# Performance work log

Hardware: AMD Instinct MI355X
Metric: run time of the kernel (lower is better)

The kernel has to match this reference:

```python
import jax, jax.numpy as jnp
import numpy as np

G, N, E = 4, 20000, 320000
D_IN = 512
# ceil(0.6*N), ceil(0.6*K1), ceil(0.5*K2) -- SAGPooling ratios 0.6, 0.6, 0.5
K1, K2, K3 = 12000, 7200, 3600
EPS = 1e-5


def setup_inputs() -> dict:
    key = jax.random.key(0)
    ks = jax.random.split(key, 32)
    def w(k, shape, fan_in):
        return jax.random.normal(k, shape, jnp.float32) / np.float32(np.sqrt(fan_in))
    inp = {
        "x": jax.random.normal(ks[0], (G, N, D_IN), jnp.float32),
        "edge_index": jax.random.randint(ks[1], (G, 2, E), 0, N, dtype=jnp.int32),
        # GCNConv weights (lin has no bias; bias added post-aggregation)
        "W1": w(ks[2], (512, 512), 512), "b1": jnp.zeros((512,), jnp.float32),
        "W2": w(ks[3], (512, 512), 512), "b2": jnp.zeros((512,), jnp.float32),
        "W3": w(ks[4], (512, 256), 512), "b3": jnp.zeros((256,), jnp.float32),
        "W4": w(ks[5], (256, 256), 256), "b4": jnp.zeros((256,), jnp.float32),
        # BatchNorm (track_running_stats=False -> always batch stats), affine params
        "g1": jnp.ones((512,), jnp.float32), "be1": jnp.zeros((512,), jnp.float32),
        "g2": jnp.ones((512,), jnp.float32), "be2": jnp.zeros((512,), jnp.float32),
        "g3": jnp.ones((256,), jnp.float32), "be3": jnp.zeros((256,), jnp.float32),
        # SAGPooling score GNN = GraphConv(d, 1): lin_rel (with bias) + lin_root (no bias)
        "p1_wrel": w(ks[6], (512, 1), 512), "p1_brel": jnp.zeros((1,), jnp.float32), "p1_wroot": w(ks[7], (512, 1), 512),
        "p2_wrel": w(ks[8], (512, 1), 512), "p2_brel": jnp.zeros((1,), jnp.float32), "p2_wroot": w(ks[9], (512, 1), 512),
        "p3_wrel": w(ks[10], (256, 1), 256), "p3_brel": jnp.zeros((1,), jnp.float32), "p3_wroot": w(ks[11], (256, 1), 256),
        "lin_w": w(ks[12], (256, 256), 256), "lin_b": jnp.zeros((256,), jnp.float32),
        "lin2_w": w(ks[13], (256, 1), 256), "lin2_b": jnp.zeros((1,), jnp.float32),
    }
    return inp


def _gcn(x, src, dst, w, W, b, n):
    # GCNConv, add_self_loops=False: deg from edge weights on target, sym-norm messages
    deg = jax.ops.segment_sum(w, dst, num_segments=n)
    dinv = jnp.where(deg > 0, jax.lax.rsqrt(jnp.where(deg > 0, deg, 1.0)), 0.0)
    norm = w * dinv[src] * dinv[dst]                       # [E]
    h = x @ W                                              # [n, d_out]
    return jax.ops.segment_sum(norm[:, None] * h[src], dst, num_segments=n) + b


def _bn(x, g, b):
    mu = jnp.mean(x, axis=0)
    var = jnp.mean((x - mu) ** 2, axis=0)
    return (x - mu) * jax.lax.rsqrt(var + EPS) * g + b


def _sag_pool(x, src, dst, w, wrel, brel, wroot, n, k):
    # score GNN = GraphConv: lin_rel(sum_j w_e x_j) + lin_root(x_i); tanh nonlinearity
    agg = jax.ops.segment_sum(w[:, None] * x[src], dst, num_segments=n)
    score = jnp.tanh((agg @ wrel + brel + x @ wroot)[:, 0])  # [n]
    top, perm = jax.lax.top_k(score, k)
    x2 = x[perm] * top[:, None]
    # filter_adj: keep edges with both endpoints selected, re-index; modeled via mask
    mapping = jnp.full((n,), -1, jnp.int32).at[perm].set(jnp.arange(k, dtype=jnp.int32))
    s2, d2 = mapping[src], mapping[dst]
    valid = (s2 >= 0) & (d2 >= 0) & (w > 0)
    return x2, jnp.maximum(s2, 0), jnp.maximum(d2, 0), valid.astype(x.dtype)


def _per_graph(x, src, dst, p):
    w = jnp.ones((E,), x.dtype)
    h = jax.nn.relu(_bn(_gcn(x, src, dst, w, p["W1"], p["b1"], N), p["g1"], p["be1"]))
    h, src, dst, w = _sag_pool(h, src, dst, w, p["p1_wrel"], p["p1_brel"], p["p1_wroot"], N, K1)
    h = jax.nn.relu(_bn(_gcn(h, src, dst, w, p["W2"], p["b2"], K1), p["g2"], p["be2"]))
    h, src, dst, w = _sag_pool(h, src, dst, w, p["p2_wrel"], p["p2_brel"], p["p2_wroot"], K1, K2)
    h = jax.nn.relu(_bn(_gcn(h, src, dst, w, p["W3"], p["b3"], K2), p["g3"], p["be3"]))
    h, src, dst, w = _sag_pool(h, src, dst, w, p["p3_wrel"], p["p3_brel"], p["p3_wroot"], K2, K3)
    h = _gcn(h, src, dst, w, p["W4"], p["b4"], K3)
    return jnp.max(h, axis=0)                               # global_max_pool, 1 graph/data


def reference(x, edge_index, W1, b1, W2, b2, W3, b3, W4, b4,
              g1, be1, g2, be2, g3, be3,
              p1_wrel, p1_brel, p1_wroot, p2_wrel, p2_brel, p2_wroot,
              p3_wrel, p3_brel, p3_wroot, lin_w, lin_b, lin2_w, lin2_b):
    p = dict(W1=W1, b1=b1, W2=W2, b2=b2, W3=W3, b3=b3, W4=W4, b4=b4,
             g1=g1, be1=be1, g2=g2, be2=be2, g3=g3, be3=be3,
             p1_wrel=p1_wrel, p1_brel=p1_brel, p1_wroot=p1_wroot,
             p2_wrel=p2_wrel, p2_brel=p2_brel, p2_wroot=p2_wroot,
             p3_wrel=p3_wrel, p3_brel=p3_brel, p3_wroot=p3_wroot)
    feats = [_per_graph(x[g], edge_index[g, 0], edge_index[g, 1], p) for g in range(G)]
    wsi = jnp.stack(feats, axis=0)                          # [G, 256] (each data has 1 graph)
    x1 = jnp.mean(wsi, axis=0, keepdims=True)               # [1, 256]
    out = jax.nn.relu(x1 @ lin_w + lin_b) @ lin2_w + lin2_b # [1, 1]
    return (out, x1)
```

## Files before the change

### kernel.cpp

```cpp
#include <hip/hip_runtime.h>

#define NGRAPH 4
#define N0 20000
#define EDG 320000
#define KP1 12000
#define KP2 7200
#define KP3 3600

typedef unsigned short u16;
typedef unsigned int u32;
typedef unsigned long long u64;
typedef short s16x8 __attribute__((ext_vector_type(8)));
typedef u16 u16x4 __attribute__((ext_vector_type(4)));
typedef u16 u16x8 __attribute__((ext_vector_type(8)));
typedef float f32x4 __attribute__((ext_vector_type(4)));

__device__ __forceinline__ float b2f(u16 v){ return __uint_as_float(((u32)v)<<16); }
__device__ __forceinline__ u16 f2bf(float f){
  u32 u=__float_as_uint(f); u32 r=(u + 0x7FFFu + ((u>>16)&1u))>>16; return (u16)r;
}

__global__ void k_probe(float* dout, int n, float code){
  int i = blockIdx.x*256 + threadIdx.x;
  if (i >= n) return;
  dout[i] = (i == 0) ? code : 12345.0f;
}

__global__ void k_zero_i32(int* p, int n){
  int i = blockIdx.x*256 + threadIdx.x;
  if (i < n) p[i] = 0;
}

__global__ void k_castw2(const float* W, u16* Wth, u16* Wtl, int K, int N){
  __shared__ float tile[32][33];
  int k0 = blockIdx.x*32, n0 = blockIdx.y*32;
  int tx = threadIdx.x & 31, ty = threadIdx.x >> 5;
  for (int r = ty; r < 32; r += 8)
    tile[r][tx] = W[(long)(k0+r)*N + n0 + tx];
  __syncthreads();
  for (int r = ty; r < 32; r += 8){
    float v = tile[tx][r];
    u16 hi = f2bf(v);
    float rs = v - b2f(hi);
    Wth[(long)(n0+r)*K + k0 + tx] = hi;
    Wtl[(long)(n0+r)*K + k0 + tx] = f2bf(rs);
  }
}

__global__ void k_edges_init(const int* ei, int* esrc, int* edst){
  int idx = blockIdx.x*256 + threadIdx.x;
  if (idx >= NGRAPH*EDG) return;
  int g = idx / EDG, e = idx - g*EDG;
  esrc[idx] = ei[(g*2+0)*EDG + e];
  edst[idx] = ei[(g*2+1)*EDG + e];
}

__global__ void k_deg(const int* esrc, const int* edst, int* deg, int n){
  int idx = blockIdx.x*256 + threadIdx.x;
  if (idx >= NGRAPH*EDG) return;
  int s = esrc[idx];
  if (s < 0) return;
  atomicAdd(&deg[(idx/EDG)*n + edst[idx]], 1);
}

__global__ void k_dinv(const int* deg, float* dinv, int ntot){
  int i = blockIdx.x*256 + threadIdx.x;
  if (i >= ntot) return;
  int d = deg[i];
  dinv[i] = (d > 0) ? rsqrtf((float)d) : 0.0f;
}

__global__ __launch_bounds__(1024) void k_scan1(const int* deg, int* offs, int* bsum, int n){
  int tid = threadIdx.x;
  int i = blockIdx.x*1024 + tid;
  __shared__ int buf[1024];
  int v = (i < n) ? deg[i] : 0;
  buf[tid] = v;
  __syncthreads();
  for (int off = 1; off < 1024; off <<= 1){
    int xv = (tid >= off) ? buf[tid-off] : 0;
    __syncthreads();
    buf[tid] += xv;
    __syncthreads();
  }
  if (i < n) offs[i] = buf[tid] - v;
  if (tid == 1023) bsum[blockIdx.x] = buf[1023];
}

__global__ __launch_bounds__(128) void k_scan2(int* bsum, int* offs, int nb, int n){
  int t = threadIdx.x;
  int v = (t < nb) ? bsum[t] : 0;
  __shared__ int buf[128];
  buf[t] = v;
  __syncthreads();
  for (int off = 1; off < 128; off <<= 1){
    int x = (t >= off) ? buf[t-off] : 0;
    __syncthreads();
    buf[t] += x;
    __syncthreads();
  }
  if (t < nb) bsum[t] = buf[t] - v;
  if (t == 127) offs[n] = buf[127];
}

__global__ __launch_bounds__(1024) void k_scan3(int* offs, const int* bsum, int n){
  int i = blockIdx.x*1024 + threadIdx.x;
  if (i < n) offs[i] += bsum[blockIdx.x];
}

__global__ void k_copy_i32(const int* a, int* b, int n){
  int i = blockIdx.x*256 + threadIdx.x;
  if (i < n) b[i] = a[i];
}

__global__ void k_csrfill(const int* esrc, const int* edst, const float* dinv,
                          int* cursor, int* csr_src, float* csr_norm, int n){
  int idx = blockIdx.x*256 + threadIdx.x;
  if (idx >= NGRAPH*EDG) return;
  int s = esrc[idx];
  if (s < 0) return;
  int g = idx/EDG;
  int d = edst[idx];
  int gs = g*n + s, gd = g*n + d;
  int pos = atomicAdd(&cursor[gd], 1);
  csr_src[pos] = gs;
  csr_norm[pos] = dinv[gs]*dinv[gd];
}

__global__ __launch_bounds__(256) void k_gemm3(const float* A, const u16* Bh_, const u16* Bl_,
                                               float* C, int K, int Nc){
  __shared__ u16 Ah[128][40];
  __shared__ u16 Al[128][40];
  __shared__ u16 Bh[128][40];
  __shared__ u16 Bl[128][40];
  const int n0 = blockIdx.x*128, m0 = blockIdx.y*128;
  const int tid = threadIdx.x, w = tid>>6, lane = tid&63;
  const int wr = w>>1, wc = w&1;
  const int fr = lane&15, fq = lane>>4;
  const int ar = tid>>3, ac = (tid&7)*4;
  const int br = tid>>2, bc = (tid&3)*8;
  f32x4 acc[4][4];
  #pragma unroll
  for (int i=0;i<4;++i)
    #pragma unroll
    for (int j=0;j<4;++j){ acc[i][j][0]=0.f; acc[i][j][1]=0.f; acc[i][j][2]=0.f; acc[i][j][3]=0.f; }
  for (int k0 = 0; k0 < K; k0 += 32){
    __syncthreads();
    #pragma unroll
    for (int i = 0; i < 4; ++i){
      int row = ar + i*32;
      float4 av = *(const float4*)(A + (long)(m0+row)*K + k0 + ac);
      float vs[4] = {av.x, av.y, av.z, av.w};
      u16x4 h, l;
      #pragma unroll
      for (int j = 0; j < 4; ++j){
        u16 hi = f2bf(vs[j]);
        h[j] = hi;
        l[j] = f2bf(vs[j] - b2f(hi));
      }
      *(u16x4*)&Ah[row][ac] = h;
      *(u16x4*)&Al[row][ac] = l;
    }
    #pragma unroll
    for (int i = 0; i < 2; ++i){
      int row = br + i*64;
      *(u16x8*)&Bh[row][bc] = *(const u16x8*)(Bh_ + (long)(n0+row)*K + k0 + bc);
      *(u16x8*)&Bl[row][bc] = *(const u16x8*)(Bl_ + (long)(n0+row)*K + k0 + bc);
    }
    __syncthreads();
    s16x8 fah[4], fal[4], fbh[4], fbl[4];
    #pragma unroll
    for (int fm = 0; fm < 4; ++fm){
      fah[fm] = *(const s16x8*)&Ah[wr*64 + fm*16 + fr][fq*8];
      fal[fm] = *(const s16x8*)&Al[wr*64 + fm*16 + fr][fq*8];
    }
    #pragma unroll
    for (int fn = 0; fn < 4; ++fn){
      fbh[fn] = *(const s16x8*)&Bh[wc*64 + fn*16 + fr][fq*8];
      fbl[fn] = *(const s16x8*)&Bl[wc*64 + fn*16 + fr][fq*8];
    }
    #pragma unroll
    for (int fm = 0; fm < 4; ++fm)
      #pragma unroll
      for (int fn = 0; fn < 4; ++fn){
        acc[fm][fn] = __builtin_amdgcn_mfma_f32_16x16x32_bf16(fal[fm], fbh[fn], acc[fm][fn], 0, 0, 0);
        acc[fm][fn] = __builtin_amdgcn_mfma_f32_16x16x32_bf16(fah[fm], fbl[fn], acc[fm][fn], 0, 0, 0);
        acc[fm][fn] = __builtin_amdgcn_mfma_f32_16x16x32_bf16(fah[fm], fbh[fn], acc[fm][fn], 0, 0, 0);
      }
  }
  #pragma unroll
  for (int fm = 0; fm < 4; ++fm){
    const int r0 = m0 + wr*64 + fm*16 + fq*4;
    #pragma unroll
    for (int fn = 0; fn < 4; ++fn){
      const int c0 = n0 + wc*64 + fn*16 + fr;
      #pragma unroll
      for (int r = 0; r < 4; ++r)
        C[(long)(r0+r)*Nc + c0] = acc[fm][fn][r];
    }
  }
}

template<int D>
__global__ void k_agg(const float* hW, const int* offs, const int* deg,
                      const int* csr_src, const float* csr_norm,
                      const float* bias, float* out, int ntot){
  int node = blockIdx.x*4 + (threadIdx.x>>6);
  if (node >= ntot) return;
  int lane = threadIdx.x & 63;
  const int V = D/256;
  f32x4 acc[V];
  #pragma unroll
  for (int j=0;j<V;++j){ acc[j][0]=0.f; acc[j][1]=0.f; acc[j][2]=0.f; acc[j][3]=0.f; }
  int p0 = offs[node], p1 = p0 + deg[node];
  for (int p = p0; p < p1; ++p) {
    int src = csr_src[p];
    float nm = csr_norm[p];
    const float* row = hW + (long)src*D + lane*4;
    #pragma unroll
    for (int j=0;j<V;++j){
      f32x4 v = *(const f32x4*)(row + j*256);
      acc[j] += nm*v;
    }
  }
  float* orow = out + (long)node*D + lane*4;
  const float* brow = bias + lane*4;
  #pragma unroll
  for (int j=0;j<V;++j){
    f32x4 b = *(const f32x4*)(brow + j*256);
    *(f32x4*)(orow + j*256) = acc[j] + b;
  }
}

template<int D>
__global__ void k_bnpart(const float* h, float* part, int n, int NB){
  int g = blockIdx.y, bx = blockIdx.x;
  int r0 = bx*256;
  int rows = n - r0; if (rows > 256) rows = 256;
  const int CPT = D/256;
  float s[CPT], q[CPT];
  #pragma unroll
  for (int j=0;j<CPT;++j){ s[j]=0.0f; q[j]=0.0f; }
  const float* base = h + ((long)g*n + r0)*D;
  for (int r = 0; r < rows; ++r)
    #pragma unroll
    for (int j=0;j<CPT;++j){
      float v = base[(long)r*D + threadIdx.x + j*256];
      s[j] += v; q[j] += v*v;
    }
  float* o = part + ((long)(g*NB + bx)*2)*D;
  #pragma unroll
  for (int j=0;j<CPT;++j){
    o[threadIdx.x + j*256]     = s[j];
    o[D + threadIdx.x + j*256] = q[j];
  }
}

__global__ void k_bnfin(const float* part, float* mean, float* rstd, int n, int D, int NB){
  int idx = blockIdx.x*256 + threadIdx.x;
  if (idx >= NGRAPH*D) return;
  int g = idx / D, c = idx - g*D;
  float s = 0.0f, q = 0.0f;
  for (int b = 0; b < NB; ++b){
    const float* o = part + ((long)(g*NB + b)*2)*D;
    s += o[c]; q += o[D + c];
  }
  float m = s/(float)n;
  float v = q/(float)n - m*m;
  mean[idx] = m;
  rstd[idx] = rsqrtf(v + 1e-5f);
}

template<int D>
__global__ void k_bnrelu_dots(float* h, const float* mean, const float* rstd,
                              const float* gam, const float* bet,
                              const float* wrel, const float* wroot,
                              float* r, float* t, int n, int ntot){
  int node = blockIdx.x*4 + (threadIdx.x>>6);
  if (node >= ntot) return;
  int lane = threadIdx.x & 63;
  int g = node / n;
  const float* mu = mean + g*D;
  const float* rs = rstd + g*D;
  float* row = h + (long)node*D;
  float sr = 0.0f, st = 0.0f;
  #pragma unroll
  for (int j = 0; j < D/64; ++j){
    int c = lane + j*64;
    float v = (row[c] - mu[c])*rs[c]*gam[c] + bet[c];
    v = fmaxf(v, 0.0f);
    row[c] = v;
    sr += v*wrel[c];
    st += v*wroot[c];
  }
  for (int o = 32; o > 0; o >>= 1){
    sr += __shfl_down(sr, o);
    st += __shfl_down(st, o);
  }
  if (lane == 0){ r[node] = sr; t[node] = st; }
}

__global__ void k_score(const float* r, const float* t, const int* offs, const int* deg,
                        const int* csr_src, const float* brel, float* score,
                        u64* keys, int n, int ntot){
  int i = blockIdx.x*256 + threadIdx.x;
  if (i >= ntot) return;
  float a = 0.0f;
  int p0 = offs[i], p1 = p0 + deg[i];
  for (int p = p0; p < p1; ++p) a += r[csr_src[p]];
  float sc = tanhf(a + brel[0] + t[i]);
  score[i] = sc;
  u32 u = __float_as_uint(sc);
  u = (u & 0x80000000u) ? ~u : (u | 0x80000000u);
  keys[i] = ((u64)u << 32) | (u64)(0xFFFFFFFFu - (u32)(i % n));
}

__global__ __launch_bounds__(1024) void k_radix(const u64* keys, u64* Tout, int n, int k){
  int g = blockIdx.x;
  const u64* kk = keys + (long)g*n;
  __shared__ u32 h0[2048];
  __shared__ u32 h1[2048];
  __shared__ u64 s_prefix;
  __shared__ int s_remaining;
  __shared__ int s_bin;
  if (threadIdx.x == 0){ s_prefix = 0ull; s_remaining = k; }
  int consumed = 0;
  for (int round = 0; round < 6; ++round){
    int nb = (round < 5) ? 11 : 9;
    int shift = 64 - consumed - nb;
    int bins = 1 << nb;
    for (int i = threadIdx.x; i < bins; i += 1024) h0[i] = 0u;
    __syncthreads();
    u64 pref = s_prefix;
    int rem = s_remaining;
    for (int i = threadIdx.x; i < n; i += 1024){
      u64 key = kk[i];
      if (consumed == 0 || (key >> (64 - consumed)) == pref)
        atomicAdd(&h0[(u32)((key >> shift) & (u64)(bins-1))], 1u);
    }
    __syncthreads();
    u32* src = h0; u32* dst = h1;
    for (int off = 1; off < bins; off <<= 1){
      for (int i = threadIdx.x; i < bins; i += 1024)
        dst[i] = src[i] + ((i + off < bins) ? src[i + off] : 0u);
      __syncthreads();
      u32* tmp = src; src = dst; dst = tmp;
    }
    for (int i = threadIdx.x; i < bins; i += 1024){
      int Sb  = (int)src[i];
      int Sb1 = (i + 1 < bins) ? (int)src[i+1] : 0;
      if (Sb >= rem && (i == bins-1 || Sb1 < rem)){
        s_bin = i;
        s_remaining = rem - Sb1;
      }
    }
    __syncthreads();
    if (threadIdx.x == 0) s_prefix = (s_prefix << nb) | (u64)s_bin;
    consumed += nb;
    __syncthreads();
  }
  if (threadIdx.x == 0) Tout[g] = s_prefix;
}

__global__ void k_select(const u64* keys, const u64* T, int* mapping,
                         int* perm, int* cnt, int n, int k, int ntot){
  int gi = blockIdx.x*256 + threadIdx.x;
  int lane = threadIdx.x & 63;
  if (gi - lane >= ntot) return;
  int g = gi / n;
  bool sel = keys[gi] >= T[g];
  u64 ball = __ballot(sel);
  u64 lt = (1ull << lane) - 1ull;
  int g0 = __shfl(g, 0);
  u64 sameg = __ballot(g == g0);
  int id = -1;
  if (g == g0){
    u64 mA = ball & sameg;
    int baseA = 0;
    if (lane == 0 && mA) baseA = atomicAdd(&cnt[g0], __popcll(mA));
    baseA = __shfl(baseA, 0);
    if (sel) id = baseA + __popcll(mA & lt);
  } else {
    u64 blanes = ~sameg;
    int firstB = (int)(__ffsll((long long)blanes) - 1);
    u64 mB = ball & blanes;
    int baseB = 0;
    if (lane == firstB && mB) baseB = atomicAdd(&cnt[g], __popcll(mB));
    baseB = __shfl(baseB, firstB);
    if (sel) id = baseB + __popcll(mB & lt);
  }
  mapping[gi] = id;
  if (id >= 0) perm[g*k + id] = gi - g*n;
}

__global__ void k_poolcopy(const float* h, const float* score, const int* perm,
                           float* outA, int n, int k, int D, int mtot){
  int m = blockIdx.x*4 + (threadIdx.x>>6);
  if (m >= mtot) return;
  int lane = threadIdx.x & 63;
  int g = m / k;
  int gi = g*n + perm[m];
  float sc = score[gi];
  const float* row = h + (long)gi*D;
  float* orow = outA + (long)m*D;
  for (int c = lane; c < D; c += 64) orow[c] = row[c]*sc;
}

__global__ void k_remap(int* esrc, int* edst, const int* mapping, int n){
  int idx = blockIdx.x*256 + threadIdx.x;
  if (idx >= NGRAPH*EDG) return;
  int s = esrc[idx];
  if (s < 0) return;
  int g = idx/EDG;
  int s2 = mapping[g*n + s], d2 = mapping[g*n + edst[idx]];
  if (s2 < 0 || d2 < 0){ esrc[idx] = -1; edst[idx] = -1; }
  else { esrc[idx] = s2; edst[idx] = d2; }
}

__global__ void k_maxpart(const float* h, float* part){
  int g = blockIdx.y, b = blockIdx.x, c = threadIdx.x;
  int r0 = b*240;
  const float* base = h + ((long)g*KP3 + r0)*256;
  float m = -3.4e38f;
  for (int r = 0; r < 240; ++r) m = fmaxf(m, base[(long)r*256 + c]);
  part[(g*15 + b)*256 + c] = m;
}

__global__ void k_maxfin(const float* part, float* feats){
  int g = blockIdx.x, c = threadIdx.x;
  float m = -3.4e38f;
  for (int b = 0; b < 15; ++b) m = fmaxf(m, part[(g*15 + b)*256 + c]);
  feats[g*256 + c] = m;
}

__global__ void k_final(const float* feats, const float* lw, const float* lb,
                        const float* l2w, const float* l2b, float* dout){
  __shared__ float sx[256];
  __shared__ float sp[256];
  int c = threadIdx.x;
  float x1 = 0.25f*(feats[c] + feats[256+c] + feats[512+c] + feats[768+c]);
  sx[c] = x1;
  __syncthreads();
  float acc = lb[c];
  for (int j = 0; j < 256; ++j) acc += sx[j]*lw[j*256 + c];
  acc = fmaxf(acc, 0.0f);
  sp[c] = acc*l2w[c];
  __syncthreads();
  for (int off = 128; off > 0; off >>= 1){
    if (c < off) sp[c] += sp[c+off];
    __syncthreads();
  }
  if (c == 0) dout[0] = sp[0] + l2b[0];
  dout[1+c] = sx[c];
}

extern "C" void kernel_launch(void* const* d_in, const int* in_sizes, int n_in,
                              void* d_out, int out_size, void* d_ws, size_t ws_size,
                              hipStream_t stream){
  const float* x  = (const float*)d_in[0];
  const int*   ei = (const int*)d_in[1];
  const float *W1 = (const float*)d_in[2],  *b1 = (const float*)d_in[3];
  const float *W2 = (const float*)d_in[4],  *b2 = (const float*)d_in[5];
  const float *W3 = (const float*)d_in[6],  *b3 = (const float*)d_in[7];
  const float *W4 = (const float*)d_in[8],  *b4 = (const float*)d_in[9];
  const float *g1 = (const float*)d_in[10], *be1 = (const float*)d_in[11];
  const float *g2 = (const float*)d_in[12], *be2 = (const float*)d_in[13];
  const float *g3 = (const float*)d_in[14], *be3 = (const float*)d_in[15];
  const float *p1r = (const float*)d_in[16], *p1b = (const float*)d_in[17], *p1o = (const float*)d_in[18];
  const float *p2r = (const float*)d_in[19], *p2b = (const float*)d_in[20], *p2o = (const float*)d_in[21];
  const float *p3r = (const float*)d_in[22], *p3b = (const float*)d_in[23], *p3o = (const float*)d_in[24];
  const float *lw = (const float*)d_in[25], *lb = (const float*)d_in[26];
  const float *l2w = (const float*)d_in[27], *l2b = (const float*)d_in[28];
  float* dout = (float*)d_out;

  bool ok = (n_in == 29) && (out_size == 257)
         && (in_sizes[0] == NGRAPH*N0*512) && (in_sizes[1] == NGRAPH*2*EDG);
  float code = ok ? (float)(ws_size >> 20) : 7777777.0f;
  k_probe<<<2,256,0,stream>>>(dout, out_size, code);
  if (!ok) return;

  char* wbase = (char*)d_ws;
  size_t woff = 0;
  auto alloc = [&](size_t bytes) -> void* {
    void* p = wbase + woff;
    woff = (woff + bytes + 255) & ~(size_t)255;
    return p;
  };
  size_t NE = (size_t)NGRAPH*N0;
  size_t RSZ = NE*512*4;
  float* R0 = (float*)alloc(RSZ);
  float* R1 = (float*)alloc(RSZ);
  u16* Wt1h = (u16*)alloc((size_t)512*512*2); u16* Wt1l = (u16*)alloc((size_t)512*512*2);
  u16* Wt2h = (u16*)alloc((size_t)512*512*2); u16* Wt2l = (u16*)alloc((size_t)512*512*2);
  u16* Wt3h = (u16*)alloc((size_t)256*512*2); u16* Wt3l = (u16*)alloc((size_t)256*512*2);
  u16* Wt4h = (u16*)alloc((size_t)256*256*2); u16* Wt4l = (u16*)alloc((size_t)256*256*2);
  int*   esrc     = (int*)  alloc((size_t)NGRAPH*EDG*4);
  int*   edst     = (int*)  alloc((size_t)NGRAPH*EDG*4);
  int*   csr_src  = (int*)  alloc((size_t)NGRAPH*EDG*4);
  float* csr_norm = (float*)alloc((size_t)NGRAPH*EDG*4);
  int*   deg      = (int*)  alloc(NE*4);
  float* dinv     = (float*)alloc(NE*4);
  int*   offs     = (int*)  alloc((NE+1)*4);
  int*   cursor   = (int*)  alloc(NE*4);
  int*   bsum     = (int*)  alloc(128*4);
  float* rbuf     = (float*)alloc(NE*4);
  float* tbuf     = (float*)alloc(NE*4);
  float* sbuf     = (float*)alloc(NE*4);
  u64*   keys     = (u64*)  alloc(NE*8);
  u64*   Tsel     = (u64*)  alloc(NGRAPH*8);
  int*   cnt      = (int*)  alloc(NGRAPH*4);
  int*   mapping  = (int*)  alloc(NE*4);
  int*   perm     = (int*)  alloc((size_t)NGRAPH*KP1*4);
  float* bnpart   = (float*)alloc((size_t)NGRAPH*79*2*512*4);
  float* bnmean   = (float*)alloc((size_t)NGRAPH*512*4);
  float* bnrstd   = (float*)alloc((size_t)NGRAPH*512*4);
  float* maxpart  = (float*)alloc((size_t)NGRAPH*15*256*4);
  float* feats    = (float*)alloc((size_t)NGRAPH*256*4);

  auto cdiv = [](long a, long b) -> int { return (int)((a + b - 1)/b); };
  long etot = (long)NGRAPH*EDG;

  {
    dim3 g1d(512/32, 512/32);
    k_castw2<<<g1d,256,0,stream>>>(W1, Wt1h, Wt1l, 512, 512);
    k_castw2<<<g1d,256,0,stream>>>(W2, Wt2h, Wt2l, 512, 512);
    dim3 g3d(512/32, 256/32);
    k_castw2<<<g3d,256,0,stream>>>(W3, Wt3h, Wt3l, 512, 256);
    dim3 g4d(256/32, 256/32);
    k_castw2<<<g4d,256,0,stream>>>(W4, Wt4h, Wt4l, 256, 256);
  }
  k_edges_init<<<cdiv(etot,256),256,0,stream>>>(ei, esrc, edst);

  struct SP { int n, din, dout_, knext; const u16 *Wh,*Wl; const float *b,*gam,*bet,*wrel,*brel,*wroot; };
  SP sp[4] = {
    {N0,  512, 512, KP1, Wt1h,Wt1l, b1,g1,be1,p1r,p1b,p1o},
    {KP1, 512, 512, KP2, Wt2h,Wt2l, b2,g2,be2,p2r,p2b,p2o},
    {KP2, 512, 256, KP3, Wt3h,Wt3l, b3,g3,be3,p3r,p3b,p3o},
    {KP3, 256, 256, 0,   Wt4h,Wt4l, b4,0,0,0,0,0},
  };

  float* bufA = R0;
  float* bufB = R1;

  for (int s = 0; s < 4; ++s){
    SP& P = sp[s];
    int ntot = NGRAPH*P.n;
    int D = P.dout_;
    const float* Ain = (s == 0) ? x : bufA;
    float* H = bufB;
    float* C = bufA;

    k_zero_i32<<<cdiv(ntot,256),256,0,stream>>>(deg, ntot);
    k_deg<<<cdiv(etot,256),256,0,stream>>>(esrc, edst, deg, P.n);
    k_dinv<<<cdiv(ntot,256),256,0,stream>>>(deg, dinv, ntot);
    {
      int nb = cdiv(ntot, 1024);
      k_scan1<<<nb,1024,0,stream>>>(deg, offs, bsum, ntot);
      k_scan2<<<1,128,0,stream>>>(bsum, offs, nb, ntot);
      k_scan3<<<nb,1024,0,stream>>>(offs, bsum, ntot);
    }
    k_copy_i32<<<cdiv(ntot,256),256,0,stream>>>(offs, cursor, ntot);
    k_csrfill<<<cdiv(etot,256),256,0,stream>>>(esrc, edst, dinv, cursor, csr_src, csr_norm, P.n);
    {
      dim3 gg(D/128, cdiv(ntot,128));
      k_gemm3<<<gg,256,0,stream>>>(Ain, P.Wh, P.Wl, H, P.din, D);
    }
    if (D == 512)
      hipLaunchKernelGGL(HIP_KERNEL_NAME(k_agg<512>), dim3(ntot/4), dim3(256), 0, stream,
                         H, offs, deg, csr_src, csr_norm, P.b, C, ntot);
    else
      hipLaunchKernelGGL(HIP_KERNEL_NAME(k_agg<256>), dim3(ntot/4), dim3(256), 0, stream,
                         H, offs, deg, csr_src, csr_norm, P.b, C, ntot);
    if (s < 3){
      int NB = cdiv(P.n, 256);
      if (D == 512)
        hipLaunchKernelGGL(HIP_KERNEL_NAME(k_bnpart<512>), dim3(NB,NGRAPH), dim3(256), 0, stream,
                           C, bnpart, P.n, NB);
      else
        hipLaunchKernelGGL(HIP_KERNEL_NAME(k_bnpart<256>), dim3(NB,NGRAPH), dim3(256), 0, stream,
                           C, bnpart, P.n, NB);
      k_bnfin<<<cdiv((long)NGRAPH*D,256),256,0,stream>>>(bnpart, bnmean, bnrstd, P.n, D, NB);
      if (D == 512)
        hipLaunchKernelGGL(HIP_KERNEL_NAME(k_bnrelu_dots<512>), dim3(ntot/4), dim3(256), 0, stream,
                           C, bnmean, bnrstd, P.gam, P.bet, P.wrel, P.wroot, rbuf, tbuf, P.n, ntot);
      else
        hipLaunchKernelGGL(HIP_KERNEL_NAME(k_bnrelu_dots<256>), dim3(ntot/4), dim3(256), 0, stream,
                           C, bnmean, bnrstd, P.gam, P.bet, P.wrel, P.wroot, rbuf, tbuf, P.n, ntot);
      k_score<<<cdiv(ntot,256),256,0,stream>>>(rbuf, tbuf, offs, deg, csr_src, P.brel, sbuf, keys, P.n, ntot);
      k_radix<<<NGRAPH,1024,0,stream>>>(keys, Tsel, P.n, P.knext);
      k_zero_i32<<<1,64,0,stream>>>(cnt, NGRAPH);
      k_select<<<cdiv(ntot,256),256,0,stream>>>(keys, Tsel, mapping, perm, cnt, P.n, P.knext, ntot);
      int mtot = NGRAPH*P.knext;
      k_poolcopy<<<mtot/4,256,0,stream>>>(C, sbuf, perm, bufB, P.n, P.knext, D, mtot);
      k_remap<<<cdiv(etot,256),256,0,stream>>>(esrc, edst, mapping, P.n);
      float* tmp = bufA; bufA = bufB; bufB = tmp;
    } else {
      k_maxpart<<<dim3(15,NGRAPH),256,0,stream>>>(C, maxpart);
      k_maxfin<<<NGRAPH,256,0,stream>>>(maxpart, feats);
      k_final<<<1,256,0,stream>>>(feats, lw, lb, l2w, l2b, dout);
    }
  }
}
```

Before: 1.883 ms.

## Derive pooled-graph CSR by filtering previous CSR instead of rebuilding from edges

```diff
diff --git a/kernel.cpp b/kernel.cpp
--- a/kernel.cpp
+++ b/kernel.cpp
@@ -58,23 +58,16 @@
 __global__ void k_deg(const int* esrc, const int* edst, int* deg, int n){
   int idx = blockIdx.x*256 + threadIdx.x;
   if (idx >= NGRAPH*EDG) return;
-  int s = esrc[idx];
-  if (s < 0) return;
   atomicAdd(&deg[(idx/EDG)*n + edst[idx]], 1);
 }
 
-__global__ void k_dinv(const int* deg, float* dinv, int ntot){
-  int i = blockIdx.x*256 + threadIdx.x;
-  if (i >= ntot) return;
-  int d = deg[i];
-  dinv[i] = (d > 0) ? rsqrtf((float)d) : 0.0f;
-}
-
-__global__ __launch_bounds__(1024) void k_scan1(const int* deg, int* offs, int* bsum, int n){
+__global__ __launch_bounds__(1024) void k_scan1(const int* deg, int* offs, int* bsum,
+                                                float* dinv, int n){
   int tid = threadIdx.x;
   int i = blockIdx.x*1024 + tid;
   __shared__ int buf[1024];
   int v = (i < n) ? deg[i] : 0;
+  if (i < n) dinv[i] = (v > 0) ? rsqrtf((float)v) : 0.0f;
   buf[tid] = v;
   __syncthreads();
   for (int off = 1; off < 1024; off <<= 1){
@@ -117,14 +110,47 @@
                           int* cursor, int* csr_src, float* csr_norm, int n){
   int idx = blockIdx.x*256 + threadIdx.x;
   if (idx >= NGRAPH*EDG) return;
-  int s = esrc[idx];
-  if (s < 0) return;
   int g = idx/EDG;
-  int d = edst[idx];
-  int gs = g*n + s, gd = g*n + d;
+  int gs = g*n + esrc[idx], gd = g*n + edst[idx];
   int pos = atomicAdd(&cursor[gd], 1);
   csr_src[pos] = gs;
   csr_norm[pos] = dinv[gs]*dinv[gd];
+}
+
+__global__ void k_filterdeg(const int* perm, const int* mapping,
+                            const int* offs_o, const int* deg_o, const int* csrs_o,
+                            int* deg_n, int n_old, int k, int mtot){
+  int m = blockIdx.x*256 + threadIdx.x;
+  if (m >= mtot) return;
+  int g = m / k;
+  int gio = g*n_old + perm[m];
+  int p0 = offs_o[gio], p1 = p0 + deg_o[gio];
+  int c = 0;
+  for (int p = p0; p < p1; ++p)
+    if (mapping[csrs_o[p]] >= 0) ++c;
+  deg_n[m] = c;
+}
+
+__global__ void k_filterfill(const int* perm, const int* mapping,
+                             const int* offs_o, const int* deg_o, const int* csrs_o,
+                             const int* offs_n, const float* dinv_n,
+                             int* csrs_n, float* csrn_n, int n_old, int k, int mtot){
+  int m = blockIdx.x*256 + threadIdx.x;
+  if (m >= mtot) return;
+  int g = m / k;
+  int gio = g*n_old + perm[m];
+  int p0 = offs_o[gio], p1 = p0 + deg_o[gio];
+  int pos = offs_n[m];
+  float dd = dinv_n[m];
+  for (int p = p0; p < p1; ++p){
+    int sm = mapping[csrs_o[p]];
+    if (sm >= 0){
+      int sg = g*k + sm;
+      csrs_n[pos] = sg;
+      csrn_n[pos] = dinv_n[sg]*dd;
+      ++pos;
+    }
+  }
 }
 
 __global__ __launch_bounds__(256) void k_gemm3(const float* A, const u16* Bh_, const u16* Bl_,
@@ -406,17 +432,6 @@
   for (int c = lane; c < D; c += 64) orow[c] = row[c]*sc;
 }
 
-__global__ void k_remap(int* esrc, int* edst, const int* mapping, int n){
-  int idx = blockIdx.x*256 + threadIdx.x;
-  if (idx >= NGRAPH*EDG) return;
-  int s = esrc[idx];
-  if (s < 0) return;
-  int g = idx/EDG;
-  int s2 = mapping[g*n + s], d2 = mapping[g*n + edst[idx]];
-  if (s2 < 0 || d2 < 0){ esrc[idx] = -1; edst[idx] = -1; }
-  else { esrc[idx] = s2; edst[idx] = d2; }
-}
-
 __global__ void k_maxpart(const float* h, float* part){
   int g = blockIdx.y, b = blockIdx.x, c = threadIdx.x;
   int r0 = b*240;
@@ -494,28 +509,32 @@
   u16* Wt2h = (u16*)alloc((size_t)512*512*2); u16* Wt2l = (u16*)alloc((size_t)512*512*2);
   u16* Wt3h = (u16*)alloc((size_t)256*512*2); u16* Wt3l = (u16*)alloc((size_t)256*512*2);
   u16* Wt4h = (u16*)alloc((size_t)256*256*2); u16* Wt4l = (u16*)alloc((size_t)256*256*2);
-  int*   esrc     = (int*)  alloc((size_t)NGRAPH*EDG*4);
-  int*   edst     = (int*)  alloc((size_t)NGRAPH*EDG*4);
-  int*   csr_src  = (int*)  alloc((size_t)NGRAPH*EDG*4);
-  float* csr_norm = (float*)alloc((size_t)NGRAPH*EDG*4);
-  int*   deg      = (int*)  alloc(NE*4);
-  float* dinv     = (float*)alloc(NE*4);
-  int*   offs     = (int*)  alloc((NE+1)*4);
-  int*   cursor   = (int*)  alloc(NE*4);
-  int*   bsum     = (int*)  alloc(128*4);
-  float* rbuf     = (float*)alloc(NE*4);
-  float* tbuf     = (float*)alloc(NE*4);
-  float* sbuf     = (float*)alloc(NE*4);
-  u64*   keys     = (u64*)  alloc(NE*8);
-  u64*   Tsel     = (u64*)  alloc(NGRAPH*8);
-  int*   cnt      = (int*)  alloc(NGRAPH*4);
-  int*   mapping  = (int*)  alloc(NE*4);
-  int*   perm     = (int*)  alloc((size_t)NGRAPH*KP1*4);
-  float* bnpart   = (float*)alloc((size_t)NGRAPH*79*2*512*4);
-  float* bnmean   = (float*)alloc((size_t)NGRAPH*512*4);
-  float* bnrstd   = (float*)alloc((size_t)NGRAPH*512*4);
-  float* maxpart  = (float*)alloc((size_t)NGRAPH*15*256*4);
-  float* feats    = (float*)alloc((size_t)NGRAPH*256*4);
+  int*   esrc  = (int*)alloc((size_t)NGRAPH*EDG*4);
+  int*   edst  = (int*)alloc((size_t)NGRAPH*EDG*4);
+  int*   csrsA = (int*)  alloc((size_t)NGRAPH*EDG*4);
+  float* csrnA = (float*)alloc((size_t)NGRAPH*EDG*4);
+  int*   csrsB = (int*)  alloc((size_t)NGRAPH*EDG*4);
+  float* csrnB = (float*)alloc((size_t)NGRAPH*EDG*4);
+  int*   degA  = (int*)  alloc(NE*4);
+  int*   degB  = (int*)  alloc(NE*4);
+  int*   offsA = (int*)  alloc((NE+1)*4);
+  int*   offsB = (int*)  alloc((NE+1)*4);
+  float* dinv  = (float*)alloc(NE*4);
+  int*   cursor= (int*)  alloc(NE*4);
+  int*   bsum  = (int*)  alloc(128*4);
+  float* rbuf  = (float*)alloc(NE*4);
+  float* tbuf  = (float*)alloc(NE*4);
+  float* sbuf  = (float*)alloc(NE*4);
+  u64*   keys  = (u64*)  alloc(NE*8);
+  u64*   Tsel  = (u64*)  alloc(NGRAPH*8);
+  int*   cnt   = (int*)  alloc(NGRAPH*4);
+  int*   mapping = (int*)alloc(NE*4);
+  int*   perm  = (int*)  alloc((size_t)NGRAPH*KP1*4);
+  float* bnpart= (float*)alloc((size_t)NGRAPH*79*2*512*4);
+  float* bnmean= (float*)alloc((size_t)NGRAPH*512*4);
+  float* bnrstd= (float*)alloc((size_t)NGRAPH*512*4);
+  float* maxpart=(float*)alloc((size_t)NGRAPH*15*256*4);
+  float* feats = (float*)alloc((size_t)NGRAPH*256*4);
 
   auto cdiv = [](long a, long b) -> int { return (int)((a + b - 1)/b); };
   long etot = (long)NGRAPH*EDG;
@@ -542,6 +561,11 @@
   float* bufA = R0;
   float* bufB = R1;
 
+  int *deg_c = degA, *offs_c = offsA, *csrs_c = csrsA;
+  float *csrn_c = csrnA;
+  int *deg_x = degB, *offs_x = offsB, *csrs_x = csrsB;
+  float *csrn_x = csrnB;
+
   for (int s = 0; s < 4; ++s){
     SP& P = sp[s];
     int ntot = NGRAPH*P.n;
@@ -549,28 +573,42 @@
     const float* Ain = (s == 0) ? x : bufA;
     float* H = bufB;
     float* C = bufA;
-
-    k_zero_i32<<<cdiv(ntot,256),256,0,stream>>>(deg, ntot);
-    k_deg<<<cdiv(etot,256),256,0,stream>>>(esrc, edst, deg, P.n);
-    k_dinv<<<cdiv(ntot,256),256,0,stream>>>(deg, dinv, ntot);
-    {
-      int nb = cdiv(ntot, 1024);
-      k_scan1<<<nb,1024,0,stream>>>(deg, offs, bsum, ntot);
-      k_scan2<<<1,128,0,stream>>>(bsum, offs, nb, ntot);
-      k_scan3<<<nb,1024,0,stream>>>(offs, bsum, ntot);
-    }
-    k_copy_i32<<<cdiv(ntot,256),256,0,stream>>>(offs, cursor, ntot);
-    k_csrfill<<<cdiv(etot,256),256,0,stream>>>(esrc, edst, dinv, cursor, csr_src, csr_norm, P.n);
+    int nb = cdiv(ntot, 1024);
+
+    if (s == 0){
+      k_zero_i32<<<cdiv(ntot,256),256,0,stream>>>(deg_c, ntot);
+      k_deg<<<cdiv(etot,256),256,0,stream>>>(esrc, edst, deg_c, P.n);
+      k_scan1<<<nb,1024,0,stream>>>(deg_c, offs_c, bsum, dinv, ntot);
+      k_scan2<<<1,128,0,stream>>>(bsum, offs_c, nb, ntot);
+      k_scan3<<<nb,1024,0,stream>>>(offs_c, bsum, ntot);
+      k_copy_i32<<<cdiv(ntot,256),256,0,stream>>>(offs_c, cursor, ntot);
+      k_csrfill<<<cdiv(etot,256),256,0,stream>>>(esrc, edst, dinv, cursor, csrs_c, csrn_c, P.n);
+    } else {
+      int n_old = sp[s-1].n;
+      k_filterdeg<<<cdiv(ntot,256),256,0,stream>>>(perm, mapping, offs_c, deg_c, csrs_c,
+                                                   deg_x, n_old, P.n, ntot);
+      k_scan1<<<nb,1024,0,stream>>>(deg_x, offs_x, bsum, dinv, ntot);
+      k_scan2<<<1,128,0,stream>>>(bsum, offs_x, nb, ntot);
+      k_scan3<<<nb,1024,0,stream>>>(offs_x, bsum, ntot);
+      k_filterfill<<<cdiv(ntot,256),256,0,stream>>>(perm, mapping, offs_c, deg_c, csrs_c,
+                                                    offs_x, dinv, csrs_x, csrn_x, n_old, P.n, ntot);
+      int* ti; float* tf;
+      ti = deg_c;  deg_c  = deg_x;  deg_x  = ti;
+      ti = offs_c; offs_c = offs_x; offs_x = ti;
+      ti = csrs_c; csrs_c = csrs_x; csrs_x = ti;
+      tf = csrn_c; csrn_c = csrn_x; csrn_x = tf;
+    }
+
     {
       dim3 gg(D/128, cdiv(ntot,128));
       k_gemm3<<<gg,256,0,stream>>>(Ain, P.Wh, P.Wl, H, P.din, D);
     }
     if (D == 512)
       hipLaunchKernelGGL(HIP_KERNEL_NAME(k_agg<512>), dim3(ntot/4), dim3(256), 0, stream,
-                         H, offs, deg, csr_src, csr_norm, P.b, C, ntot);
+                         H, offs_c, deg_c, csrs_c, csrn_c, P.b, C, ntot);
     else
       hipLaunchKernelGGL(HIP_KERNEL_NAME(k_agg<256>), dim3(ntot/4), dim3(256), 0, stream,
-                         H, offs, deg, csr_src, csr_norm, P.b, C, ntot);
+                         H, offs_c, deg_c, csrs_c, csrn_c, P.b, C, ntot);
     if (s < 3){
       int NB = cdiv(P.n, 256);
       if (D == 512)
@@ -586,13 +624,13 @@
       else
         hipLaunchKernelGGL(HIP_KERNEL_NAME(k_bnrelu_dots<256>), dim3(ntot/4), dim3(256), 0, stream,
                            C, bnmean, bnrstd, P.gam, P.bet, P.wrel, P.wroot, rbuf, tbuf, P.n, ntot);
-      k_score<<<cdiv(ntot,256),256,0,stream>>>(rbuf, tbuf, offs, deg, csr_src, P.brel, sbuf, keys, P.n, ntot);
+      k_score<<<cdiv(ntot,256),256,0,stream>>>(rbuf, tbuf, offs_c, deg_c, csrs_c, P.brel,
+                                               sbuf, keys, P.n, ntot);
       k_radix<<<NGRAPH,1024,0,stream>>>(keys, Tsel, P.n, P.knext);
       k_zero_i32<<<1,64,0,stream>>>(cnt, NGRAPH);
       k_select<<<cdiv(ntot,256),256,0,stream>>>(keys, Tsel, mapping, perm, cnt, P.n, P.knext, ntot);
       int mtot = NGRAPH*P.knext;
       k_poolcopy<<<mtot/4,256,0,stream>>>(C, sbuf, perm, bufB, P.n, P.knext, D, mtot);
-      k_remap<<<cdiv(etot,256),256,0,stream>>>(esrc, edst, mapping, P.n);
       float* tmp = bufA; bufA = bufB; bufB = tmp;
     } else {
       k_maxpart<<<dim3(15,NGRAPH),256,0,stream>>>(C, maxpart);
```

After: 1.814 ms. 1.04x faster.
